# Kernel tuning notes

Measured on AMD Instinct MI355X. Metric: run time of the kernel, lower is better.

## Reference

```python
import jax, jax.numpy as jnp
import numpy as np

N_NODES = 100000
NUM_LAYER = 3
REG_WEIGHT = 1e-4


def setup_inputs() -> dict:
    key = jax.random.key(0)
    ks = jax.random.split(key, 6)
    E = 1280000
    B = 4096
    D = 64
    # xavier-uniform-like scale for embedding table
    emb_weight = jax.random.normal(ks[0], (N_NODES, D), dtype=jnp.float32) * 0.01
    src = jax.random.randint(ks[1], (E,), 0, N_NODES, dtype=jnp.int32)
    dst = jax.random.randint(ks[2], (E,), 0, N_NODES, dtype=jnp.int32)
    users = jax.random.randint(ks[3], (B,), 0, N_NODES, dtype=jnp.int32)
    pos = jax.random.randint(ks[4], (B,), 0, N_NODES, dtype=jnp.int32)
    neg = jax.random.randint(ks[5], (B,), 0, N_NODES, dtype=jnp.int32)
    return {"emb_weight": emb_weight, "src": src, "dst": dst,
            "users": users, "pos": pos, "neg": neg}


def _edge_norm(src, dst):
    # DGL norm(): d = sum of edge mask (ones) per dst node; adj_e = d[src]^-0.5 * d[dst]^-0.5
    ones = jnp.ones(src.shape[0], dtype=jnp.float32)
    deg = jax.ops.segment_sum(ones, dst, num_segments=N_NODES)
    dinv = jnp.where(deg > 0, deg ** -0.5, 0.0)  # inf -> 0 handling
    return dinv[src] * dinv[dst]  # [E]


def _propagate(emb_weight, src, dst, adj):
    # LightGCN propagation: h_{l+1}[v] = sum_{(u->v)} adj_e * h_l[u]
    h = emb_weight
    layers = [h]
    for _ in range(NUM_LAYER):
        m = h[src] * adj[:, None]                    # [E, D] gather + edge weight
        h = jax.ops.segment_sum(m, dst, num_segments=N_NODES)  # [N, D] scatter-sum
        layers.append(h)
    return jnp.mean(jnp.stack(layers, axis=1), axis=1)  # mean over L+1 layers


def reference(emb_weight, src, dst, users, pos, neg):
    adj = _edge_norm(src, dst)
    all_emb = _propagate(emb_weight, src, dst, adj)

    u_e, p_e, n_e = all_emb[users], all_emb[pos], all_emb[neg]
    u0, p0, n0 = emb_weight[users], emb_weight[pos], emb_weight[neg]

    B = users.shape[0]
    reg_loss = 0.5 * (jnp.sum(u0 ** 2) + jnp.sum(p0 ** 2) + jnp.sum(n0 ** 2)) / B
    reg_loss = reg_loss * REG_WEIGHT

    pos_scores = jnp.sum(u_e * p_e, axis=1)
    neg_scores = jnp.sum(u_e * n_e, axis=1)
    loss_emb = jnp.mean(jax.nn.softplus(neg_scores - pos_scores))

    loss = loss_emb + reg_loss
    return loss, loss_emb, reg_loss
```

## Files before the change

### kernel.cpp

```cpp
#include <hip/hip_runtime.h>
#include <hip/hip_fp8.h>
#include <math.h>

#define N_NODES 100000
#define DIM 64
#define NUM_LAYER 3
#define BATCH 4096
#define REG_WEIGHT 1e-4f
#define NBUCKET 391
#define STAGE_CAP 4096
#define CURPAD 16
#define H_SCALE 256.0f
#define H_INV_SCALE (1.0f / 256.0f)

typedef float floatx2 __attribute__((ext_vector_type(2)));

__device__ unsigned char g_hf8[2][(size_t)N_NODES * DIM];
__device__ float g_sums[(size_t)3 * BATCH * DIM];
__device__ int   g_row_ptr[N_NODES + 1];
__device__ float g_dinv[N_NODES];
__device__ int   g_bcur[NBUCKET * CURPAD];
__device__ unsigned int g_stage[NBUCKET * STAGE_CAP];
__device__ int   g_csr[1280000];
__device__ int   g_shead[N_NODES];
__device__ int   g_snext[3 * BATCH];
__device__ float g_part_sp[BATCH];
__device__ float g_part_rg[BATCH];

__device__ inline void fma4_fp8(unsigned int d, float w,
                                float& a0, float& a1, float& a2, float& a3) {
    floatx2 lo = __builtin_amdgcn_cvt_pk_f32_fp8((int)d, false);
    floatx2 hi = __builtin_amdgcn_cvt_pk_f32_fp8((int)d, true);
    a0 = fmaf(w, lo.x, a0); a1 = fmaf(w, lo.y, a1);
    a2 = fmaf(w, hi.x, a2); a3 = fmaf(w, hi.y, a3);
}
__device__ inline unsigned int pack4_fp8(float a0, float a1, float a2, float a3) {
    int w = __builtin_amdgcn_cvt_pk_fp8_f32(a0, a1, 0, false);
    w     = __builtin_amdgcn_cvt_pk_fp8_f32(a2, a3, w, true);
    return (unsigned int)w;
}

#define EDGES_PER_THREAD 4
__global__ void __launch_bounds__(1024) stage_buckets(const int* __restrict__ src,
                                                      const int* __restrict__ dst, int E,
                                                      const int* __restrict__ users,
                                                      const int* __restrict__ pos,
                                                      const int* __restrict__ neg) {
    __shared__ int h[NBUCKET];
    __shared__ int cur[NBUCKET];
    int tid = threadIdx.x;
    int gt = blockIdx.x * 1024 + tid;
    if (gt < 3 * BATCH) {
        int which = gt / BATCH, s = gt - which * BATCH;
        const int* idx = (which == 0) ? users : ((which == 1) ? pos : neg);
        g_snext[gt] = atomicExch(&g_shead[idx[s]], gt + 1);
    }
    int base = blockIdx.x * (1024 * EDGES_PER_THREAD);
    for (int i = tid; i < NBUCKET; i += 1024) h[i] = 0;
    __syncthreads();
    int myd[EDGES_PER_THREAD], mys[EDGES_PER_THREAD];
    #pragma unroll
    for (int k = 0; k < EDGES_PER_THREAD; ++k) {
        int e = base + k * 1024 + tid;
        if (e < E) {
            myd[k] = dst[e]; mys[k] = src[e];
            atomicAdd(&h[myd[k] >> 8], 1);
        } else myd[k] = -1;
    }
    __syncthreads();
    for (int i = tid; i < NBUCKET; i += 1024) {
        int c = h[i];
        cur[i] = c ? (atomicAdd(&g_bcur[i * CURPAD], c) + i * STAGE_CAP) : 0;
    }
    __syncthreads();
    #pragma unroll
    for (int k = 0; k < EDGES_PER_THREAD; ++k) {
        if (myd[k] >= 0) {
            int p = atomicAdd(&cur[myd[k] >> 8], 1);
            g_stage[p] = (unsigned int)((mys[k] << 8) | (myd[k] & 255));
        }
    }
}

__global__ void __launch_bounds__(512) finalize_place(const float* __restrict__ emb) {
    __shared__ int cs[512];
    __shared__ int lh[256], sc[256], cur[256];
    __shared__ float ldv[256];
    int b = blockIdx.x, t = threadIdx.x;
    int c = (t < NBUCKET) ? g_bcur[t * CURPAD] : 0;
    cs[t] = c;
    __syncthreads();
    for (int off = 1; off < 512; off <<= 1) {
        int x = (t >= off) ? cs[t - off] : 0;
        __syncthreads();
        cs[t] += x;
        __syncthreads();
    }
    int mybase = (b > 0) ? cs[b - 1] : 0;
    int cnt    = cs[b] - mybase;
    if (b == 0 && t == 0) g_row_ptr[N_NODES] = cs[NBUCKET - 1];
    int sbeg = b * STAGE_CAP;
    if (t < 256) lh[t] = 0;
    __syncthreads();
    for (int k = t; k < cnt; k += 512)
        atomicAdd(&lh[g_stage[sbeg + k] & 255], 1);
    __syncthreads();
    int v = 0;
    if (t < 256) { v = lh[t]; sc[t] = v; }
    __syncthreads();
    for (int off = 1; off < 256; off <<= 1) {
        int x = (t >= off && t < 256) ? sc[t - off] : 0;
        __syncthreads();
        if (t < 256) sc[t] += x;
        __syncthreads();
    }
    if (t < 256) {
        int start = mybase + sc[t] - v;
        cur[t] = start;
        float dv = (v > 0) ? rsqrtf((float)v) : 0.0f;
        ldv[t] = dv;
        int node = (b << 8) + t;
        if (node < N_NODES) {
            g_row_ptr[node] = start;
            g_dinv[node]    = dv;
        }
    }
    __syncthreads();
    for (int k = t; k < cnt; k += 512) {
        unsigned int e = g_stage[sbeg + k];
        int pos = atomicAdd(&cur[e & 255], 1);
        g_csr[pos] = (int)(e >> 8);
    }
    {
        int nbase = b << 8;
        int rows = N_NODES - nbase; if (rows > 256) rows = 256;
        unsigned int* hw = (unsigned int*)g_hf8[0];
        for (int idx = t; idx < rows * 16; idx += 512) {
            int row = idx >> 4, li = idx & 15;
            const float4 ev = *(const float4*)(emb + (size_t)(nbase + row) * DIM + li * 4);
            float s = ldv[row] * H_SCALE;
            hw[(size_t)(nbase + row) * 16 + li] =
                pack4_fp8(ev.x * s, ev.y * s, ev.z * s, ev.w * s);
        }
    }
}

__global__ void pull_layer_fp8(const unsigned char* __restrict__ h,
                               unsigned char* __restrict__ hn, int mode) {
    int gid0 = blockIdx.x * blockDim.x + threadIdx.x;
    if (mode == 1 && gid0 < NBUCKET) g_bcur[gid0 * CURPAD] = 0;
    int wid  = gid0 >> 6;
    int lane = threadIdx.x & 63;
    int g  = lane >> 4;
    int li = lane & 15;
    int n = wid * 4 + g;
    if (n >= N_NODES) return;
    int beg = g_row_ptr[n], end = g_row_ptr[n + 1];
    float dinvN = g_dinv[n];
    float a0 = 0.f, a1 = 0.f, a2 = 0.f, a3 = 0.f;
    for (int k = beg; k < end; k += 4) {
        int k1 = min(k + 1, end - 1);
        int k2 = min(k + 2, end - 1);
        int k3 = min(k + 3, end - 1);
        int s0 = g_csr[k];
        int s1 = g_csr[k1];
        int s2 = g_csr[k2];
        int s3 = g_csr[k3];
        unsigned int d0 = *(const unsigned int*)(h + (size_t)s0 * DIM + li * 4);
        unsigned int d1 = *(const unsigned int*)(h + (size_t)s1 * DIM + li * 4);
        unsigned int d2 = *(const unsigned int*)(h + (size_t)s2 * DIM + li * 4);
        unsigned int d3 = *(const unsigned int*)(h + (size_t)s3 * DIM + li * 4);
        float w1 = (k + 1 < end) ? 1.0f : 0.0f;
        float w2 = (k + 2 < end) ? 1.0f : 0.0f;
        float w3 = (k + 3 < end) ? 1.0f : 0.0f;
        fma4_fp8(d0, 1.0f, a0, a1, a2, a3);
        fma4_fp8(d1, w1, a0, a1, a2, a3);
        fma4_fp8(d2, w2, a0, a1, a2, a3);
        fma4_fp8(d3, w3, a0, a1, a2, a3);
    }
    float dd = dinvN * dinvN;
    *(unsigned int*)(hn + (size_t)n * DIM + li * 4) =
        pack4_fp8(a0 * dd, a1 * dd, a2 * dd, a3 * dd);
    if (mode) {
        float gw = dinvN * H_INV_SCALE;
        int sidx = g_shead[n];
        while (sidx > 0) {
            int sr = sidx - 1;
            float* sp = &g_sums[(size_t)sr * DIM + li * 4];
            if (mode == 1) {
                sp[0] = a0 * gw; sp[1] = a1 * gw;
                sp[2] = a2 * gw; sp[3] = a3 * gw;
            } else {
                sp[0] += a0 * gw; sp[1] += a1 * gw;
                sp[2] += a2 * gw; sp[3] += a3 * gw;
            }
            sidx = g_snext[sr];
        }
        if (mode == 2 && li == 0) g_shead[n] = 0;
    }
}

__global__ void pull_sampled(const unsigned char* __restrict__ h,
                             const int* __restrict__ users, const int* __restrict__ pos,
                             const int* __restrict__ neg) {
    int gid0 = blockIdx.x * blockDim.x + threadIdx.x;
    int wid  = gid0 >> 6;
    int lane = threadIdx.x & 63;
    int g  = lane >> 4;
    int li = lane & 15;
    int s = wid * 4 + g;
    if (s >= 3 * BATCH) return;
    int which = s >> 12;
    int i     = s & (BATCH - 1);
    const int* idx = (which == 0) ? users : ((which == 1) ? pos : neg);
    int node = idx[i];
    int beg = g_row_ptr[node], end = g_row_ptr[node + 1];
    float dinvN = g_dinv[node];
    float a0 = 0.f, a1 = 0.f, a2 = 0.f, a3 = 0.f;
    for (int k = beg; k < end; k += 4) {
        int k1 = min(k + 1, end - 1);
        int k2 = min(k + 2, end - 1);
        int k3 = min(k + 3, end - 1);
        int s0 = g_csr[k];
        int s1 = g_csr[k1];
        int s2 = g_csr[k2];
        int s3 = g_csr[k3];
        unsigned int d0 = *(const unsigned int*)(h + (size_t)s0 * DIM + li * 4);
        unsigned int d1 = *(const unsigned int*)(h + (size_t)s1 * DIM + li * 4);
        unsigned int d2 = *(const unsigned int*)(h + (size_t)s2 * DIM + li * 4);
        unsigned int d3 = *(const unsigned int*)(h + (size_t)s3 * DIM + li * 4);
        float w1 = (k + 1 < end) ? 1.0f : 0.0f;
        float w2 = (k + 2 < end) ? 1.0f : 0.0f;
        float w3 = (k + 3 < end) ? 1.0f : 0.0f;
        fma4_fp8(d0, 1.0f, a0, a1, a2, a3);
        fma4_fp8(d1, w1, a0, a1, a2, a3);
        fma4_fp8(d2, w2, a0, a1, a2, a3);
        fma4_fp8(d3, w3, a0, a1, a2, a3);
    }
    float gw = dinvN * H_INV_SCALE;
    float* sp = &g_sums[(size_t)s * DIM + li * 4];
    sp[0] += a0 * gw;
    sp[1] += a1 * gw;
    sp[2] += a2 * gw;
    sp[3] += a3 * gw;
}

__global__ void score_reduce(const float* __restrict__ emb,
                             const int* __restrict__ users, const int* __restrict__ pos,
                             const int* __restrict__ neg) {
    int wid  = (blockIdx.x * blockDim.x + threadIdx.x) >> 6;
    int lane = threadIdx.x & 63;
    if (wid >= BATCH) return;
    float u0 = emb[(size_t)users[wid] * DIM + lane];
    float p0 = emb[(size_t)pos[wid]   * DIM + lane];
    float n0 = emb[(size_t)neg[wid]   * DIM + lane];
    float u = 0.25f * (g_sums[(size_t)wid * DIM + lane] + u0);
    float p = 0.25f * (g_sums[(size_t)(BATCH + wid) * DIM + lane] + p0);
    float n = 0.25f * (g_sums[(size_t)(2 * BATCH + wid) * DIM + lane] + n0);
    float ps = u * p;
    float ns = u * n;
    float rg = u0 * u0 + p0 * p0 + n0 * n0;
    #pragma unroll
    for (int off = 32; off > 0; off >>= 1) {
        ps += __shfl_down(ps, off);
        ns += __shfl_down(ns, off);
        rg += __shfl_down(rg, off);
    }
    if (lane == 0) {
        float x  = ns - ps;
        float sp = fmaxf(x, 0.0f) + log1pf(expf(-fabsf(x)));
        g_part_sp[wid] = sp;
        g_part_rg[wid] = rg;
    }
}

__global__ void final_reduce(float* __restrict__ out) {
    __shared__ float s_sp[256], s_rg[256];
    int t = threadIdx.x;
    float sp = 0.0f, rg = 0.0f;
    for (int i = t; i < BATCH; i += 256) { sp += g_part_sp[i]; rg += g_part_rg[i]; }
    s_sp[t] = sp; s_rg[t] = rg;
    __syncthreads();
    for (int off = 128; off > 0; off >>= 1) {
        if (t < off) { s_sp[t] += s_sp[t + off]; s_rg[t] += s_rg[t + off]; }
        __syncthreads();
    }
    if (t == 0) {
        float loss_emb = s_sp[0] / (float)BATCH;
        float reg      = 0.5f * s_rg[0] / (float)BATCH * REG_WEIGHT;
        out[0] = loss_emb + reg;
        out[1] = loss_emb;
        out[2] = reg;
    }
}

extern "C" void kernel_launch(void* const* d_in, const int* in_sizes, int n_in,
                              void* d_out, int out_size, void* d_ws, size_t ws_size,
                              hipStream_t stream) {
    const float* emb   = (const float*)d_in[0];
    const int*   src   = (const int*)d_in[1];
    const int*   dst   = (const int*)d_in[2];
    const int*   users = (const int*)d_in[3];
    const int*   pos   = (const int*)d_in[4];
    const int*   neg   = (const int*)d_in[5];
    const int E = in_sizes[1];
    float* out = (float*)d_out;

    unsigned char* hf_a;  hipGetSymbolAddress((void**)&hf_a, HIP_SYMBOL(g_hf8));
    unsigned char* hf_b = hf_a + (size_t)N_NODES * DIM;

    const int STAGE_BLOCKS = (E + 1024 * EDGES_PER_THREAD - 1) / (1024 * EDGES_PER_THREAD);
    stage_buckets<<<STAGE_BLOCKS, 1024, 0, stream>>>(src, dst, E, users, pos, neg);
    finalize_place<<<NBUCKET, 512, 0, stream>>>(emb);

    const int NQUAD = (N_NODES + 3) / 4;
    const int PULL_BLOCKS = (NQUAD * 64 + 255) / 256;

    pull_layer_fp8<<<PULL_BLOCKS, 256, 0, stream>>>(hf_a, hf_b, 1);

    pull_layer_fp8<<<PULL_BLOCKS, 256, 0, stream>>>(hf_b, hf_a, 2);

    const int SAMP_BLOCKS = ((3 * BATCH + 3) / 4 * 64 + 255) / 256;
    pull_sampled<<<SAMP_BLOCKS, 256, 0, stream>>>(hf_a, users, pos, neg);

    score_reduce<<<(BATCH * 64 + 255) / 256, 256, 0, stream>>>(emb, users, pos, neg);
    final_reduce<<<1, 256, 0, stream>>>(out);
}
```

Measured before the change: 185.4 us.

## Build CSR via global degree atomics and scan instead of bucket staging

Replaces the two-pass bucketed staging CSR construction with a direct approach: global atomic degree count per destination, a per-block scan (each block re-sums all prior degrees) that also converts embeddings to fp8, then a placement pass with per-node atomic cursors. Row pointers become cursor-end values, so pull kernels read beg/end from g_cend after placement. This removes the staging buffer and the bucket-local shared-memory sort, but adds an extra kernel launch, heavy global atomics on 100k counters, and O(N) redundant prefix summing per block. Edge order within a row becomes nondeterministic.

```diff
diff --git a/kernel.cpp b/kernel.cpp
--- a/kernel.cpp
+++ b/kernel.cpp
@@ -8,8 +8,6 @@
 #define BATCH 4096
 #define REG_WEIGHT 1e-4f
 #define NBUCKET 391
-#define STAGE_CAP 4096
-#define CURPAD 16
 #define H_SCALE 256.0f
 #define H_INV_SCALE (1.0f / 256.0f)
 
@@ -17,10 +15,9 @@
 
 __device__ unsigned char g_hf8[2][(size_t)N_NODES * DIM];
 __device__ float g_sums[(size_t)3 * BATCH * DIM];
-__device__ int   g_row_ptr[N_NODES + 1];
+__device__ int   g_deg[N_NODES];
+__device__ int   g_cend[N_NODES];
 __device__ float g_dinv[N_NODES];
-__device__ int   g_bcur[NBUCKET * CURPAD];
-__device__ unsigned int g_stage[NBUCKET * STAGE_CAP];
 __device__ int   g_csr[1280000];
 __device__ int   g_shead[N_NODES];
 __device__ int   g_snext[3 * BATCH];
@@ -40,73 +37,39 @@
     return (unsigned int)w;
 }
 
-#define EDGES_PER_THREAD 4
-__global__ void __launch_bounds__(1024) stage_buckets(const int* __restrict__ src,
-                                                      const int* __restrict__ dst, int E,
-                                                      const int* __restrict__ users,
-                                                      const int* __restrict__ pos,
-                                                      const int* __restrict__ neg) {
-    __shared__ int h[NBUCKET];
-    __shared__ int cur[NBUCKET];
-    int tid = threadIdx.x;
-    int gt = blockIdx.x * 1024 + tid;
+__global__ void __launch_bounds__(1024) deg_chains(const int* __restrict__ dst, int E,
+                                                   const int* __restrict__ users,
+                                                   const int* __restrict__ pos,
+                                                   const int* __restrict__ neg) {
+    int gt = blockIdx.x * 1024 + threadIdx.x;
     if (gt < 3 * BATCH) {
         int which = gt / BATCH, s = gt - which * BATCH;
         const int* idx = (which == 0) ? users : ((which == 1) ? pos : neg);
         g_snext[gt] = atomicExch(&g_shead[idx[s]], gt + 1);
     }
-    int base = blockIdx.x * (1024 * EDGES_PER_THREAD);
-    for (int i = tid; i < NBUCKET; i += 1024) h[i] = 0;
-    __syncthreads();
-    int myd[EDGES_PER_THREAD], mys[EDGES_PER_THREAD];
-    #pragma unroll
-    for (int k = 0; k < EDGES_PER_THREAD; ++k) {
-        int e = base + k * 1024 + tid;
-        if (e < E) {
-            myd[k] = dst[e]; mys[k] = src[e];
-            atomicAdd(&h[myd[k] >> 8], 1);
-        } else myd[k] = -1;
-    }
-    __syncthreads();
-    for (int i = tid; i < NBUCKET; i += 1024) {
-        int c = h[i];
-        cur[i] = c ? (atomicAdd(&g_bcur[i * CURPAD], c) + i * STAGE_CAP) : 0;
-    }
-    __syncthreads();
-    #pragma unroll
-    for (int k = 0; k < EDGES_PER_THREAD; ++k) {
-        if (myd[k] >= 0) {
-            int p = atomicAdd(&cur[myd[k] >> 8], 1);
-            g_stage[p] = (unsigned int)((mys[k] << 8) | (myd[k] & 255));
-        }
-    }
-}
-
-__global__ void __launch_bounds__(512) finalize_place(const float* __restrict__ emb) {
-    __shared__ int cs[512];
-    __shared__ int lh[256], sc[256], cur[256];
+    int stride = gridDim.x * 1024;
+    for (int e = gt; e < E; e += stride)
+        atomicAdd(&g_deg[dst[e]], 1);
+}
+
+__global__ void __launch_bounds__(512) scan_convert(const float* __restrict__ emb) {
+    __shared__ int red[512];
+    __shared__ int sc[256];
     __shared__ float ldv[256];
     int b = blockIdx.x, t = threadIdx.x;
-    int c = (t < NBUCKET) ? g_bcur[t * CURPAD] : 0;
-    cs[t] = c;
-    __syncthreads();
-    for (int off = 1; off < 512; off <<= 1) {
-        int x = (t >= off) ? cs[t - off] : 0;
-        __syncthreads();
-        cs[t] += x;
-        __syncthreads();
-    }
-    int mybase = (b > 0) ? cs[b - 1] : 0;
-    int cnt    = cs[b] - mybase;
-    if (b == 0 && t == 0) g_row_ptr[N_NODES] = cs[NBUCKET - 1];
-    int sbeg = b * STAGE_CAP;
-    if (t < 256) lh[t] = 0;
-    __syncthreads();
-    for (int k = t; k < cnt; k += 512)
-        atomicAdd(&lh[g_stage[sbeg + k] & 255], 1);
-    __syncthreads();
+    int nbase = b << 8;
+    int rows = N_NODES - nbase; if (rows > 256) rows = 256;
+    int sum = 0;
+    for (int i = t; i < nbase; i += 512) sum += g_deg[i];
+    red[t] = sum;
+    __syncthreads();
+    for (int off = 256; off > 0; off >>= 1) {
+        if (t < off) red[t] += red[t + off];
+        __syncthreads();
+    }
+    int bbase = red[0];
     int v = 0;
-    if (t < 256) { v = lh[t]; sc[t] = v; }
+    if (t < 256) { v = (t < rows) ? g_deg[nbase + t] : 0; sc[t] = v; }
     __syncthreads();
     for (int off = 1; off < 256; off <<= 1) {
         int x = (t >= off && t < 256) ? sc[t - off] : 0;
@@ -114,48 +77,45 @@
         if (t < 256) sc[t] += x;
         __syncthreads();
     }
-    if (t < 256) {
-        int start = mybase + sc[t] - v;
-        cur[t] = start;
+    if (t < rows) {
+        g_cend[nbase + t] = bbase + sc[t] - v;
         float dv = (v > 0) ? rsqrtf((float)v) : 0.0f;
         ldv[t] = dv;
-        int node = (b << 8) + t;
-        if (node < N_NODES) {
-            g_row_ptr[node] = start;
-            g_dinv[node]    = dv;
-        }
-    }
-    __syncthreads();
-    for (int k = t; k < cnt; k += 512) {
-        unsigned int e = g_stage[sbeg + k];
-        int pos = atomicAdd(&cur[e & 255], 1);
-        g_csr[pos] = (int)(e >> 8);
-    }
-    {
-        int nbase = b << 8;
-        int rows = N_NODES - nbase; if (rows > 256) rows = 256;
-        unsigned int* hw = (unsigned int*)g_hf8[0];
-        for (int idx = t; idx < rows * 16; idx += 512) {
-            int row = idx >> 4, li = idx & 15;
-            const float4 ev = *(const float4*)(emb + (size_t)(nbase + row) * DIM + li * 4);
-            float s = ldv[row] * H_SCALE;
-            hw[(size_t)(nbase + row) * 16 + li] =
-                pack4_fp8(ev.x * s, ev.y * s, ev.z * s, ev.w * s);
-        }
+        g_dinv[nbase + t] = dv;
+    }
+    __syncthreads();
+    unsigned int* hw = (unsigned int*)g_hf8[0];
+    for (int idx = t; idx < rows * 16; idx += 512) {
+        int row = idx >> 4, li = idx & 15;
+        const float4 ev = *(const float4*)(emb + (size_t)(nbase + row) * DIM + li * 4);
+        float s = ldv[row] * H_SCALE;
+        hw[(size_t)(nbase + row) * 16 + li] =
+            pack4_fp8(ev.x * s, ev.y * s, ev.z * s, ev.w * s);
+    }
+}
+
+__global__ void __launch_bounds__(1024) place(const int* __restrict__ src,
+                                              const int* __restrict__ dst, int E) {
+    int gt = blockIdx.x * 1024 + threadIdx.x;
+    int stride = gridDim.x * 1024;
+    for (int i = gt; i < N_NODES; i += stride) g_deg[i] = 0;
+    for (int e = gt; e < E; e += stride) {
+        int p = atomicAdd(&g_cend[dst[e]], 1);
+        g_csr[p] = src[e];
     }
 }
 
 __global__ void pull_layer_fp8(const unsigned char* __restrict__ h,
                                unsigned char* __restrict__ hn, int mode) {
     int gid0 = blockIdx.x * blockDim.x + threadIdx.x;
-    if (mode == 1 && gid0 < NBUCKET) g_bcur[gid0 * CURPAD] = 0;
     int wid  = gid0 >> 6;
     int lane = threadIdx.x & 63;
     int g  = lane >> 4;
     int li = lane & 15;
     int n = wid * 4 + g;
     if (n >= N_NODES) return;
-    int beg = g_row_ptr[n], end = g_row_ptr[n + 1];
+    int end = g_cend[n];
+    int beg = (n > 0) ? g_cend[n - 1] : 0;
     float dinvN = g_dinv[n];
     float a0 = 0.f, a1 = 0.f, a2 = 0.f, a3 = 0.f;
     for (int k = beg; k < end; k += 4) {
@@ -214,7 +174,8 @@
     int i     = s & (BATCH - 1);
     const int* idx = (which == 0) ? users : ((which == 1) ? pos : neg);
     int node = idx[i];
-    int beg = g_row_ptr[node], end = g_row_ptr[node + 1];
+    int end = g_cend[node];
+    int beg = (node > 0) ? g_cend[node - 1] : 0;
     float dinvN = g_dinv[node];
     float a0 = 0.f, a1 = 0.f, a2 = 0.f, a3 = 0.f;
     for (int k = beg; k < end; k += 4) {
@@ -309,9 +270,10 @@
     unsigned char* hf_a;  hipGetSymbolAddress((void**)&hf_a, HIP_SYMBOL(g_hf8));
     unsigned char* hf_b = hf_a + (size_t)N_NODES * DIM;
 
-    const int STAGE_BLOCKS = (E + 1024 * EDGES_PER_THREAD - 1) / (1024 * EDGES_PER_THREAD);
-    stage_buckets<<<STAGE_BLOCKS, 1024, 0, stream>>>(src, dst, E, users, pos, neg);
-    finalize_place<<<NBUCKET, 512, 0, stream>>>(emb);
+    const int EDGE_BLOCKS = (E + 4095) / 4096;
+    deg_chains<<<EDGE_BLOCKS, 1024, 0, stream>>>(dst, E, users, pos, neg);
+    scan_convert<<<NBUCKET, 512, 0, stream>>>(emb);
+    place<<<EDGE_BLOCKS, 1024, 0, stream>>>(src, dst, E);
 
     const int NQUAD = (N_NODES + 3) / 4;
     const int PULL_BLOCKS = (NQUAD * 64 + 255) / 256;
```

After: 335.7 us. +81.1%, slower.
